# Kernel tuning notes

Hardware: AMD Instinct MI355X
Metric: run time of the kernel (lower is better)

Reference implementation:

```python
import jax, jax.numpy as jnp
import numpy as np

MARGIN = 0.5
HIERARCHY_LEVEL = 0
EPS = 1e-05


def setup_inputs() -> dict:
    key = jax.random.key(0)
    k1, k2, k3, k4 = jax.random.split(key, 4)
    n, m, d, L, n_classes = 4096, 32768, 128, 2, 100
    embeddings = jax.random.normal(k1, (n, d), dtype=jnp.float32)
    ref_embeddings = jax.random.normal(k2, (m, d), dtype=jnp.float32)
    labels = jax.random.randint(k3, (n, L), 0, n_classes, dtype=jnp.int64)
    ref_labels = jax.random.randint(k4, (m, L), 0, n_classes, dtype=jnp.int64)
    return {"embeddings": embeddings, "labels": labels,
            "ref_embeddings": ref_embeddings, "ref_labels": ref_labels}


def reference(embeddings, labels, ref_embeddings, ref_labels):
    # select hierarchy level
    lab = labels[:, HIERARCHY_LEVEL]          # [n]
    ref_lab = ref_labels[:, HIERARCHY_LEVEL]  # [m]
    n = embeddings.shape[0]
    sim = embeddings @ ref_embeddings.T       # [n, m]
    same = lab[:, None] == ref_lab[None, :]   # [n, m] bool
    # positive pairs: same label and sim < 1 - eps -> contribute (1 - sim)
    pos_mask = same & (sim < 1.0 - EPS)
    # negative pairs: different label and sim > margin -> contribute sim
    neg_mask = (~same) & (sim > MARGIN)
    pos_loss = jnp.sum(jnp.where(pos_mask, 1.0 - sim, 0.0))
    neg_loss = jnp.sum(jnp.where(neg_mask, sim, 0.0))
    return (pos_loss + neg_loss) / n
```

## Files before the change

kernel.cpp:

```cpp
#include <hip/hip_runtime.h>
#include <stdint.h>

#define N_EMB 4096
#define M_REF 32768
#define D_K   128
#define BM    128
#define BN    128
#define NCOLTILES 16
#define COLCHUNK (BN * NCOLTILES)
#define NCCHUNK (M_REF / COLCHUNK)
#define NROWT  (N_EMB / BM)

typedef __attribute__((ext_vector_type(8))) short short8;
typedef __attribute__((ext_vector_type(4))) float float4v;

static __device__ __forceinline__ unsigned short f2bf(float f) {
    unsigned int u = __builtin_bit_cast(unsigned int, f);
    u += 0x7FFFu + ((u >> 16) & 1u);
    return (unsigned short)(u >> 16);
}

#define CVT_THREADS (768 * 256)

__global__ void cvt_kernel(const float* __restrict__ emb, const float* __restrict__ ref,
                           unsigned short* __restrict__ aw, unsigned short* __restrict__ bw,
                           float* __restrict__ out) {
    const int NA4 = N_EMB * D_K / 4;
    int i0 = blockIdx.x * blockDim.x + threadIdx.x;
    if (i0 == 0) *out = 0.0f;
    #pragma unroll
    for (int k = 0; k < 6; ++k) {
        int i = i0 + k * CVT_THREADS;
        const float4* src;
        unsigned short* dst;
        int j;
        if (i < NA4) { src = (const float4*)emb; dst = aw; j = i; }
        else         { src = (const float4*)ref; dst = bw; j = i - NA4; }
        float4 v = src[j];
        ushort4 o;
        o.x = f2bf(v.x); o.y = f2bf(v.y); o.z = f2bf(v.z); o.w = f2bf(v.w);
        *(ushort4*)(dst + (size_t)j * 4) = o;
    }
}

static __device__ __forceinline__ void gld_lds16(const void* g, void* l) {
    __builtin_amdgcn_global_load_lds((__attribute__((address_space(1))) void*)g,
                                     (__attribute__((address_space(3))) void*)l,
                                     16, 0, 0);
}
static __device__ __forceinline__ void gld_lds4(const void* g, void* l) {
    __builtin_amdgcn_global_load_lds((__attribute__((address_space(1))) void*)g,
                                     (__attribute__((address_space(3))) void*)l,
                                     4, 0, 0);
}

static __device__ __forceinline__ void stage_tile(const unsigned short* __restrict__ g,
                                                  unsigned short* lbuf, int tid) {
    const int rbase = tid >> 4;
    const int ch    = tid & 15;
    const int sc    = ch ^ rbase;
    const char* g0 = (const char*)g + ((size_t)rbase * D_K + sc * 8) * 2;
    char* l0 = (char*)lbuf + (size_t)tid * 16;
    #pragma unroll
    for (int i = 0; i < 8; ++i)
        gld_lds16(g0 + (size_t)i * (16 * D_K * 2), l0 + i * 4096);
}

static __device__ __forceinline__ void stage_labels(const int* __restrict__ rlab,
                                                    int col0, int* lsm, int tid) {
    const char* g0 = (const char*)rlab + ((size_t)col0 * 2 + (size_t)tid * 2) * 4;
    char* l0 = (char*)lsm + (size_t)tid * 4;
    #pragma unroll
    for (int i = 0; i < 8; ++i)
        gld_lds4(g0 + (size_t)i * 2048, l0 + i * 1024);
}

static __device__ __forceinline__ void compute_tile(
    const unsigned short* __restrict__ bp,
    const short8 a_reg[4][4], const int b_off[16],
    const int labv[4][4], const int* __restrict__ rl_t,
    int wn, int l15, float lsum[4])
{
    float4v acc[4][4] = {};
    #pragma unroll
    for (int ks = 0; ks < 4; ++ks) {
        short8 b_reg[4];
        #pragma unroll
        for (int nt = 0; nt < 4; ++nt)
            b_reg[nt] = *(const short8*)((const char*)bp + b_off[ks * 4 + nt]);
        #pragma unroll
        for (int mt = 0; mt < 4; ++mt)
            #pragma unroll
            for (int nt = 0; nt < 4; ++nt)
                acc[mt][nt] = __builtin_amdgcn_mfma_f32_16x16x32_bf16(
                    a_reg[mt][ks], b_reg[nt], acc[mt][nt], 0, 0, 0);
    }

    int rl[4];
    #pragma unroll
    for (int nt = 0; nt < 4; ++nt)
        rl[nt] = rl_t[wn * 64 + nt * 16 + l15];

    #pragma unroll
    for (int mt = 0; mt < 4; ++mt)
        #pragma unroll
        for (int nt = 0; nt < 4; ++nt)
            #pragma unroll
            for (int r = 0; r < 4; ++r) {
                float s = acc[mt][nt][r];
                float pos = fmaxf(1.0f - s, 0.0f);
                float neg = (s > 0.5f) ? s : 0.0f;
                lsum[r] += (labv[mt][r] == rl[nt]) ? pos : neg;
            }
}

__launch_bounds__(256, 2)
__global__ void xbm_kernel(const unsigned short* __restrict__ aw,
                           const unsigned short* __restrict__ bw,
                           const int* __restrict__ lab,
                           const int* __restrict__ rlab,
                           float* __restrict__ out) {
    __shared__ unsigned short b_sm[2][BN * D_K];
    __shared__ int rl_sm[COLCHUNK];
    __shared__ float red_sm[4];

    const int tid  = threadIdx.x;
    const int lane = tid & 63;
    const int wave = tid >> 6;
    const int wm = wave >> 1, wn = wave & 1;
    const int quad = lane >> 4;
    const int l15  = lane & 15;

    const int rtile  = blockIdx.x >> 4;
    const int cchunk = blockIdx.x & 15;
    const int row0 = rtile * BM;
    const int col0 = cchunk * COLCHUNK;

    stage_tile(aw + (size_t)row0 * D_K, b_sm[0], tid);
    stage_tile(bw + (size_t)col0 * D_K, b_sm[1], tid);
    stage_labels(rlab, col0, rl_sm, tid);

    int labv[4][4];
    #pragma unroll
    for (int mt = 0; mt < 4; ++mt)
        #pragma unroll
        for (int r = 0; r < 4; ++r)
            labv[mt][r] = lab[(row0 + wm * 64 + mt * 16 + quad * 4 + r) * 2];

    __syncthreads();

    short8 a_reg[4][4];
    #pragma unroll
    for (int mt = 0; mt < 4; ++mt) {
        int ml = wm * 64 + mt * 16 + l15;
        #pragma unroll
        for (int ks = 0; ks < 4; ++ks) {
            int cs = (ks * 4 + quad) ^ l15;
            a_reg[mt][ks] = *(const short8*)(b_sm[0] + (size_t)ml * D_K + cs * 8);
        }
    }

    int b_off[16];
    #pragma unroll
    for (int ks = 0; ks < 4; ++ks)
        #pragma unroll
        for (int nt = 0; nt < 4; ++nt) {
            int nl = wn * 64 + nt * 16 + l15;
            int cs = (ks * 4 + quad) ^ l15;
            b_off[ks * 4 + nt] = (nl * D_K + cs * 8) * 2;
        }

    float lsum[4] = {0.0f, 0.0f, 0.0f, 0.0f};

    __syncthreads();

    #pragma unroll 1
    for (int t = 0; t < NCOLTILES; t += 2) {
        stage_tile(bw + (size_t)(col0 + (t + 1) * BN) * D_K, b_sm[0], tid);
        compute_tile(b_sm[1], a_reg, b_off, labv, rl_sm + t * BN, wn, l15, lsum);
        __syncthreads();

        if (t + 2 < NCOLTILES)
            stage_tile(bw + (size_t)(col0 + (t + 2) * BN) * D_K, b_sm[1], tid);
        compute_tile(b_sm[0], a_reg, b_off, labv, rl_sm + (t + 1) * BN, wn, l15, lsum);
        __syncthreads();
    }

    float loss = (lsum[0] + lsum[1]) + (lsum[2] + lsum[3]);
    #pragma unroll
    for (int off = 32; off > 0; off >>= 1)
        loss += __shfl_down(loss, off, 64);
    if (lane == 0) red_sm[wave] = loss;
    __syncthreads();
    if (tid == 0) {
        float v = (red_sm[0] + red_sm[1] + red_sm[2] + red_sm[3]) * (1.0f / (float)N_EMB);
        atomicAdd(out, v);
    }
}

extern "C" void kernel_launch(void* const* d_in, const int* in_sizes, int n_in,
                              void* d_out, int out_size, void* d_ws, size_t ws_size,
                              hipStream_t stream) {
    const float* emb     = (const float*)d_in[0];
    const int*   labels  = (const int*)d_in[1];
    const float* ref     = (const float*)d_in[2];
    const int*   rlabels = (const int*)d_in[3];
    float* out = (float*)d_out;

    unsigned short* aw = (unsigned short*)d_ws;
    unsigned short* bw = aw + (size_t)N_EMB * D_K;

    cvt_kernel<<<768, 256, 0, stream>>>(emb, ref, aw, bw, out);
    xbm_kernel<<<NROWT * NCCHUNK, 256, 0, stream>>>(aw, bw, labels, rlabels, out);
}
```

Measured before the change: 118.7 us.

## Split loss into label-free negative sum plus per-class gathered correction

The main GEMM tiles now accumulate only the negative term (s > 0.5) for every pair, with no per-element label comparison. A bucketing pass in the conversion kernel groups rows and columns by class, and extra blocks compute a gathered per-class GEMM that adds the positive term and subtracts the negative term for same-label pairs. This removes label loads and compare/select work from the hot epilogue. It also shrinks tiles to BN=64 with 32 rows per wave to raise occupancy, at the cost of a small serial histogram/scatter block and roughly 1% extra gathered GEMM work. The 1 - s clamp is used in place of the s < 1 - eps test, and NCLS=100 is hardcoded to match the label range.

New measurement: 182.0 us. 53.3% more time.

```diff
diff --git a/kernel.cpp b/kernel.cpp
--- a/kernel.cpp
+++ b/kernel.cpp
@@ -4,12 +4,14 @@
 #define N_EMB 4096
 #define M_REF 32768
 #define D_K   128
+#define NCLS  100
 #define BM    128
-#define BN    128
-#define NCOLTILES 16
-#define COLCHUNK (BN * NCOLTILES)
+#define BN    64
+#define NT_PER 16
+#define COLCHUNK (BN * NT_PER)
 #define NCCHUNK (M_REF / COLCHUNK)
 #define NROWT  (N_EMB / BM)
+#define XBLOCKS (NROWT * NCCHUNK)
 
 typedef __attribute__((ext_vector_type(8))) short short8;
 typedef __attribute__((ext_vector_type(4))) float float4v;
@@ -20,177 +22,222 @@
     return (unsigned short)(u >> 16);
 }
 
-#define CVT_THREADS (768 * 256)
-
-__global__ void cvt_kernel(const float* __restrict__ emb, const float* __restrict__ ref,
-                           unsigned short* __restrict__ aw, unsigned short* __restrict__ bw,
-                           float* __restrict__ out) {
-    const int NA4 = N_EMB * D_K / 4;
-    int i0 = blockIdx.x * blockDim.x + threadIdx.x;
-    if (i0 == 0) *out = 0.0f;
-    #pragma unroll
-    for (int k = 0; k < 6; ++k) {
-        int i = i0 + k * CVT_THREADS;
-        const float4* src;
-        unsigned short* dst;
-        int j;
-        if (i < NA4) { src = (const float4*)emb; dst = aw; j = i; }
-        else         { src = (const float4*)ref; dst = bw; j = i - NA4; }
-        float4 v = src[j];
-        ushort4 o;
-        o.x = f2bf(v.x); o.y = f2bf(v.y); o.z = f2bf(v.z); o.w = f2bf(v.w);
-        *(ushort4*)(dst + (size_t)j * 4) = o;
-    }
-}
-
 static __device__ __forceinline__ void gld_lds16(const void* g, void* l) {
     __builtin_amdgcn_global_load_lds((__attribute__((address_space(1))) void*)g,
                                      (__attribute__((address_space(3))) void*)l,
                                      16, 0, 0);
 }
-static __device__ __forceinline__ void gld_lds4(const void* g, void* l) {
-    __builtin_amdgcn_global_load_lds((__attribute__((address_space(1))) void*)g,
-                                     (__attribute__((address_space(3))) void*)l,
-                                     4, 0, 0);
-}
-
-static __device__ __forceinline__ void stage_tile(const unsigned short* __restrict__ g,
-                                                  unsigned short* lbuf, int tid) {
-    const int rbase = tid >> 4;
-    const int ch    = tid & 15;
-    const int sc    = ch ^ rbase;
-    const char* g0 = (const char*)g + ((size_t)rbase * D_K + sc * 8) * 2;
-    char* l0 = (char*)lbuf + (size_t)tid * 16;
+
+#define CVT_THREADS (768 * 256)
+
+__global__ void cvt_kernel(const float* __restrict__ emb, const float* __restrict__ ref,
+                           unsigned short* __restrict__ aw, unsigned short* __restrict__ bw,
+                           const int* __restrict__ lab, const int* __restrict__ rlab,
+                           int* __restrict__ cnt_row, int* __restrict__ cnt_col,
+                           int* __restrict__ base_row, int* __restrict__ base_col,
+                           int* __restrict__ rowidx, int* __restrict__ colidx,
+                           float* __restrict__ out) {
+    const int tid = threadIdx.x;
+    if (blockIdx.x < 768) {
+        const int NA4 = N_EMB * D_K / 4;
+        int i0 = blockIdx.x * 256 + tid;
+        if (i0 == 0) *out = 0.0f;
+        #pragma unroll
+        for (int k = 0; k < 6; ++k) {
+            int i = i0 + k * CVT_THREADS;
+            const float4* src;
+            unsigned short* dst;
+            int j;
+            if (i < NA4) { src = (const float4*)emb; dst = aw; j = i; }
+            else         { src = (const float4*)ref; dst = bw; j = i - NA4; }
+            float4 v = src[j];
+            ushort4 o;
+            o.x = f2bf(v.x); o.y = f2bf(v.y); o.z = f2bf(v.z); o.w = f2bf(v.w);
+            *(ushort4*)(dst + (size_t)j * 4) = o;
+        }
+    } else {
+        __shared__ int hr[NCLS], hc[NCLS], orw[NCLS], ocl[NCLS];
+        for (int c = tid; c < NCLS; c += 256) { hr[c] = 0; hc[c] = 0; }
+        __syncthreads();
+        for (int i = tid; i < N_EMB; i += 256) atomicAdd(&hr[lab[i * 2]], 1);
+        for (int j = tid; j < M_REF; j += 256) atomicAdd(&hc[rlab[j * 2]], 1);
+        __syncthreads();
+        if (tid == 0) {
+            int rb = 0, cb = 0;
+            for (int c = 0; c < NCLS; ++c) {
+                orw[c] = rb; base_row[c] = rb; cnt_row[c] = hr[c]; rb += hr[c];
+                ocl[c] = cb; base_col[c] = cb; cnt_col[c] = hc[c]; cb += hc[c];
+            }
+        }
+        __syncthreads();
+        for (int i = tid; i < N_EMB; i += 256) {
+            int c = lab[i * 2];
+            rowidx[atomicAdd(&orw[c], 1)] = i;
+        }
+        for (int j = tid; j < M_REF; j += 256) {
+            int c = rlab[j * 2];
+            colidx[atomicAdd(&ocl[c], 1)] = j;
+        }
+    }
+}
+
+template<int NI>
+static __device__ __forceinline__ void stage_rows(const unsigned short* __restrict__ g,
+                                                  unsigned short* l, int tid) {
+    const int rlow = tid >> 4;
+    const int sc   = (tid & 15) ^ rlow;
+    const char* g0 = (const char*)g + (rlow * D_K + sc * 8) * 2;
+    char* l0 = (char*)l + tid * 16;
     #pragma unroll
-    for (int i = 0; i < 8; ++i)
+    for (int i = 0; i < NI; ++i)
         gld_lds16(g0 + (size_t)i * (16 * D_K * 2), l0 + i * 4096);
 }
 
-static __device__ __forceinline__ void stage_labels(const int* __restrict__ rlab,
-                                                    int col0, int* lsm, int tid) {
-    const char* g0 = (const char*)rlab + ((size_t)col0 * 2 + (size_t)tid * 2) * 4;
-    char* l0 = (char*)lsm + (size_t)tid * 4;
+static __device__ __forceinline__ void stage_gather(const unsigned short* __restrict__ base,
+                                                    const int* __restrict__ idxlist, int count,
+                                                    unsigned short* l, int tid) {
+    const int rlow = tid >> 4;
+    const int sc   = (tid & 15) ^ rlow;
+    char* l0 = (char*)l + tid * 16;
     #pragma unroll
-    for (int i = 0; i < 8; ++i)
-        gld_lds4(g0 + (size_t)i * 2048, l0 + i * 1024);
-}
-
-static __device__ __forceinline__ void compute_tile(
-    const unsigned short* __restrict__ bp,
-    const short8 a_reg[4][4], const int b_off[16],
-    const int labv[4][4], const int* __restrict__ rl_t,
-    int wn, int l15, float lsum[4])
-{
-    float4v acc[4][4] = {};
-    #pragma unroll
-    for (int ks = 0; ks < 4; ++ks) {
-        short8 b_reg[4];
-        #pragma unroll
-        for (int nt = 0; nt < 4; ++nt)
-            b_reg[nt] = *(const short8*)((const char*)bp + b_off[ks * 4 + nt]);
-        #pragma unroll
-        for (int mt = 0; mt < 4; ++mt)
-            #pragma unroll
-            for (int nt = 0; nt < 4; ++nt)
-                acc[mt][nt] = __builtin_amdgcn_mfma_f32_16x16x32_bf16(
-                    a_reg[mt][ks], b_reg[nt], acc[mt][nt], 0, 0, 0);
-    }
-
-    int rl[4];
-    #pragma unroll
-    for (int nt = 0; nt < 4; ++nt)
-        rl[nt] = rl_t[wn * 64 + nt * 16 + l15];
-
-    #pragma unroll
-    for (int mt = 0; mt < 4; ++mt)
-        #pragma unroll
-        for (int nt = 0; nt < 4; ++nt)
-            #pragma unroll
-            for (int r = 0; r < 4; ++r) {
-                float s = acc[mt][nt][r];
-                float pos = fmaxf(1.0f - s, 0.0f);
-                float neg = (s > 0.5f) ? s : 0.0f;
-                lsum[r] += (labv[mt][r] == rl[nt]) ? pos : neg;
-            }
-}
-
-__launch_bounds__(256, 2)
+    for (int i = 0; i < 4; ++i) {
+        int r = i * 16 + rlow;
+        if (r < count) {
+            int gi = idxlist[r];
+            gld_lds16((const char*)base + ((size_t)gi * D_K + sc * 8) * 2, l0 + i * 4096);
+        }
+    }
+}
+
+__launch_bounds__(256, 4)
 __global__ void xbm_kernel(const unsigned short* __restrict__ aw,
                            const unsigned short* __restrict__ bw,
-                           const int* __restrict__ lab,
-                           const int* __restrict__ rlab,
+                           const int* __restrict__ cnt_row, const int* __restrict__ cnt_col,
+                           const int* __restrict__ base_row, const int* __restrict__ base_col,
+                           const int* __restrict__ rowidx, const int* __restrict__ colidx,
                            float* __restrict__ out) {
     __shared__ unsigned short b_sm[2][BN * D_K];
-    __shared__ int rl_sm[COLCHUNK];
     __shared__ float red_sm[4];
 
     const int tid  = threadIdx.x;
     const int lane = tid & 63;
     const int wave = tid >> 6;
-    const int wm = wave >> 1, wn = wave & 1;
     const int quad = lane >> 4;
     const int l15  = lane & 15;
 
-    const int rtile  = blockIdx.x >> 4;
-    const int cchunk = blockIdx.x & 15;
-    const int row0 = rtile * BM;
-    const int col0 = cchunk * COLCHUNK;
-
-    stage_tile(aw + (size_t)row0 * D_K, b_sm[0], tid);
-    stage_tile(bw + (size_t)col0 * D_K, b_sm[1], tid);
-    stage_labels(rlab, col0, rl_sm, tid);
-
-    int labv[4][4];
-    #pragma unroll
-    for (int mt = 0; mt < 4; ++mt)
+    float bsum = 0.0f;
+
+    if (blockIdx.x < XBLOCKS) {
+        const int rtile  = blockIdx.x >> 5;
+        const int cchunk = blockIdx.x & 31;
+        const int row0 = rtile * BM;
+        const int col0 = cchunk * COLCHUNK;
+
+        stage_rows<8>(aw + (size_t)row0 * D_K, &b_sm[0][0], tid);
+        __syncthreads();
+
+        short8 a_reg[2][4];
         #pragma unroll
-        for (int r = 0; r < 4; ++r)
-            labv[mt][r] = lab[(row0 + wm * 64 + mt * 16 + quad * 4 + r) * 2];
-
-    __syncthreads();
-
-    short8 a_reg[4][4];
-    #pragma unroll
-    for (int mt = 0; mt < 4; ++mt) {
-        int ml = wm * 64 + mt * 16 + l15;
-        #pragma unroll
-        for (int ks = 0; ks < 4; ++ks) {
-            int cs = (ks * 4 + quad) ^ l15;
-            a_reg[mt][ks] = *(const short8*)(b_sm[0] + (size_t)ml * D_K + cs * 8);
-        }
-    }
-
-    int b_off[16];
-    #pragma unroll
-    for (int ks = 0; ks < 4; ++ks)
-        #pragma unroll
-        for (int nt = 0; nt < 4; ++nt) {
-            int nl = wn * 64 + nt * 16 + l15;
-            int cs = (ks * 4 + quad) ^ l15;
-            b_off[ks * 4 + nt] = (nl * D_K + cs * 8) * 2;
-        }
-
-    float lsum[4] = {0.0f, 0.0f, 0.0f, 0.0f};
-
-    __syncthreads();
-
-    #pragma unroll 1
-    for (int t = 0; t < NCOLTILES; t += 2) {
-        stage_tile(bw + (size_t)(col0 + (t + 1) * BN) * D_K, b_sm[0], tid);
-        compute_tile(b_sm[1], a_reg, b_off, labv, rl_sm + t * BN, wn, l15, lsum);
-        __syncthreads();
-
-        if (t + 2 < NCOLTILES)
-            stage_tile(bw + (size_t)(col0 + (t + 2) * BN) * D_K, b_sm[1], tid);
-        compute_tile(b_sm[0], a_reg, b_off, labv, rl_sm + (t + 1) * BN, wn, l15, lsum);
-        __syncthreads();
-    }
-
-    float loss = (lsum[0] + lsum[1]) + (lsum[2] + lsum[3]);
+        for (int mt = 0; mt < 2; ++mt) {
+            int ml = wave * 32 + mt * 16 + l15;
+            #pragma unroll
+            for (int ks = 0; ks < 4; ++ks) {
+                int cs = (ks * 4 + quad) ^ l15;
+                a_reg[mt][ks] = *(const short8*)(&b_sm[0][0] + (size_t)ml * D_K + cs * 8);
+            }
+        }
+        __syncthreads();
+
+        stage_rows<4>(bw + (size_t)col0 * D_K, b_sm[0], tid);
+
+        float lsum[4] = {0.0f, 0.0f, 0.0f, 0.0f};
+
+        #define COMPUTE_TILE(BP)                                                  \
+            {                                                                     \
+                const unsigned short* bp_ = (BP);                                 \
+                float4v acc[2][4] = {};                                           \
+                _Pragma("unroll")                                                 \
+                for (int ks = 0; ks < 4; ++ks) {                                  \
+                    short8 breg[4];                                               \
+                    _Pragma("unroll")                                             \
+                    for (int nt = 0; nt < 4; ++nt) {                              \
+                        int nl = nt * 16 + l15;                                   \
+                        int cs = (ks * 4 + quad) ^ l15;                           \
+                        breg[nt] = *(const short8*)(bp_ + (size_t)nl * D_K + cs * 8); \
+                    }                                                             \
+                    _Pragma("unroll")                                             \
+                    for (int mt = 0; mt < 2; ++mt)                                \
+                        _Pragma("unroll")                                         \
+                        for (int nt = 0; nt < 4; ++nt)                            \
+                            acc[mt][nt] = __builtin_amdgcn_mfma_f32_16x16x32_bf16(\
+                                a_reg[mt][ks], breg[nt], acc[mt][nt], 0, 0, 0);   \
+                }                                                                 \
+                _Pragma("unroll")                                                 \
+                for (int mt = 0; mt < 2; ++mt)                                    \
+                    _Pragma("unroll")                                             \
+                    for (int nt = 0; nt < 4; ++nt)                                \
+                        _Pragma("unroll")                                         \
+                        for (int r = 0; r < 4; ++r) {                             \
+                            float s = acc[mt][nt][r];                             \
+                            lsum[r] += (s > 0.5f) ? s : 0.0f;                     \
+                        }                                                         \
+            }
+
+        #pragma unroll 1
+        for (int t = 0; t < NT_PER; t += 2) {
+            __syncthreads();
+            stage_rows<4>(bw + (size_t)(col0 + (t + 1) * BN) * D_K, b_sm[1], tid);
+            COMPUTE_TILE(b_sm[0]);
+            __syncthreads();
+            if (t + 2 < NT_PER)
+                stage_rows<4>(bw + (size_t)(col0 + (t + 2) * BN) * D_K, b_sm[0], tid);
+            COMPUTE_TILE(b_sm[1]);
+        }
+        bsum = (lsum[0] + lsum[1]) + (lsum[2] + lsum[3]);
+    } else {
+        const int cls = blockIdx.x - XBLOCKS;
+        const int rn = cnt_row[cls], cn = cnt_col[cls];
+        const int rb = base_row[cls], cb = base_col[cls];
+
+        for (int r0 = 0; r0 < rn; r0 += 64) {
+            const int rch = min(64, rn - r0);
+            __syncthreads();
+            stage_gather(aw, rowidx + rb + r0, rch, b_sm[0], tid);
+            for (int c0 = 0; c0 < cn; c0 += 64) {
+                const int cch = min(64, cn - c0);
+                __syncthreads();
+                stage_gather(bw, colidx + cb + c0, cch, b_sm[1], tid);
+                __syncthreads();
+                const int slot = wave * 16 + l15;
+                const bool cvalid = slot < cch;
+                #pragma unroll 1
+                for (int mt = 0; mt < 4; ++mt) {
+                    if (mt * 16 >= rch) break;
+                    float4v acc = {0.0f, 0.0f, 0.0f, 0.0f};
+                    #pragma unroll
+                    for (int ks = 0; ks < 4; ++ks) {
+                        int cs = (ks * 4 + quad) ^ l15;
+                        short8 a = *(const short8*)(b_sm[0] + (size_t)(mt * 16 + l15) * D_K + cs * 8);
+                        short8 b = *(const short8*)(b_sm[1] + (size_t)slot * D_K + cs * 8);
+                        acc = __builtin_amdgcn_mfma_f32_16x16x32_bf16(a, b, acc, 0, 0, 0);
+                    }
+                    #pragma unroll
+                    for (int r = 0; r < 4; ++r) {
+                        int m_loc = mt * 16 + quad * 4 + r;
+                        if (cvalid && m_loc < rch) {
+                            float s = acc[r];
+                            bsum += fmaxf(1.0f - s, 0.0f) - ((s > 0.5f) ? s : 0.0f);
+                        }
+                    }
+                }
+            }
+        }
+    }
+
     #pragma unroll
     for (int off = 32; off > 0; off >>= 1)
-        loss += __shfl_down(loss, off, 64);
-    if (lane == 0) red_sm[wave] = loss;
+        bsum += __shfl_down(bsum, off, 64);
+    if (lane == 0) red_sm[wave] = bsum;
     __syncthreads();
     if (tid == 0) {
         float v = (red_sm[0] + red_sm[1] + red_sm[2] + red_sm[3]) * (1.0f / (float)N_EMB);
@@ -207,9 +254,21 @@
     const int*   rlabels = (const int*)d_in[3];
     float* out = (float*)d_out;
 
-    unsigned short* aw = (unsigned short*)d_ws;
-    unsigned short* bw = aw + (size_t)N_EMB * D_K;
-
-    cvt_kernel<<<768, 256, 0, stream>>>(emb, ref, aw, bw, out);
-    xbm_kernel<<<NROWT * NCCHUNK, 256, 0, stream>>>(aw, bw, labels, rlabels, out);
-}
+    char* ws = (char*)d_ws;
+    unsigned short* aw = (unsigned short*)ws;
+    unsigned short* bw = (unsigned short*)(ws + (1u << 20));
+    int* cnt_row  = (int*)(ws + 0x900000);
+    int* cnt_col  = (int*)(ws + 0x900200);
+    int* base_row = (int*)(ws + 0x900400);
+    int* base_col = (int*)(ws + 0x900600);
+    int* rowidx   = (int*)(ws + 0x900800);
+    int* colidx   = (int*)(ws + 0x904800);
+
+    cvt_kernel<<<769, 256, 0, stream>>>(emb, ref, aw, bw,
+                                        (const int*)labels, (const int*)rlabels,
+                                        cnt_row, cnt_col, base_row, base_col,
+                                        rowidx, colidx, out);
+    xbm_kernel<<<XBLOCKS + NCLS, 256, 0, stream>>>(aw, bw,
+                                                   cnt_row, cnt_col, base_row, base_col,
+                                                   rowidx, colidx, out);
+}
```
